# Performance work log

Hardware: AMD Instinct MI355X
Metric: run time of the kernel (lower is better)

## Reference

```python
import jax, jax.numpy as jnp
import numpy as np

H = 16          # n_heads
DH = 128        # head_dim
DR = 64         # rope_dim
DC = DH - DR    # content_dim = 64
THETA = 10000.0
SCALE = 1.0 / np.sqrt(DH)


def _rope_tables(T, dtype):
    inv = 1.0 / (THETA ** (jnp.arange(0, DR, 2, dtype=jnp.float32) / DR))  # [DR/2]
    t = jnp.arange(T, dtype=jnp.float32)
    freqs = jnp.outer(t, inv)  # [T, DR/2]
    return jnp.cos(freqs).astype(dtype), jnp.sin(freqs).astype(dtype)


def _apply_rope(x, cos, sin):
    # x: [B,H,T,DR]; cos/sin: [T,DR/2] broadcast over B,H
    d = x.shape[-1] // 2
    x1, x2 = x[..., :d], x[..., d:]
    return jnp.concatenate([x1 * cos - x2 * sin, x1 * sin + x2 * cos], axis=-1)


def setup_inputs() -> dict:
    key = jax.random.key(0)
    ks = jax.random.split(key, 9)
    B, T, D = 1, 2048, 2048
    s = 0.02
    return {
        "x": jax.random.normal(ks[0], (B, T, D), jnp.float32),
        "Wq_down": jax.random.normal(ks[1], (D, 512), jnp.float32) * s,
        "Wq_up": jax.random.normal(ks[2], (512, H * DC), jnp.float32) * s,
        "Wq_rope": jax.random.normal(ks[3], (D, H * DR), jnp.float32) * s,
        "Wkv_down": jax.random.normal(ks[4], (D, 512), jnp.float32) * s,
        "Wk_up": jax.random.normal(ks[5], (512, H * DC), jnp.float32) * s,
        "Wv_up": jax.random.normal(ks[6], (512, H * DH), jnp.float32) * s,
        "Wk_rope": jax.random.normal(ks[7], (D, H * DR), jnp.float32) * s,
        "Wo": jax.random.normal(ks[8], (H * DH, D), jnp.float32) * s,
    }


def reference(x, Wq_down, Wq_up, Wq_rope, Wkv_down, Wk_up, Wv_up, Wk_rope, Wo):
    B, T, D = x.shape
    # low-rank query path: down then up, content part only
    q_content = ((x @ Wq_down) @ Wq_up).reshape(B, T, H, DC).transpose(0, 2, 1, 3)
    q_pos = (x @ Wq_rope).reshape(B, T, H, DR).transpose(0, 2, 1, 3)
    kv_latent = x @ Wkv_down                    # [B,T,d_latent]
    k_pos = (x @ Wk_rope).reshape(B, T, H, DR).transpose(0, 2, 1, 3)

    cos, sin = _rope_tables(T, x.dtype)
    q_pos = _apply_rope(q_pos, cos, sin)
    k_pos = _apply_rope(k_pos, cos, sin)

    k_content = (kv_latent @ Wk_up).reshape(B, T, H, DC).transpose(0, 2, 1, 3)
    v = (kv_latent @ Wv_up).reshape(B, T, H, DH).transpose(0, 2, 1, 3)

    q = jnp.concatenate([q_content, q_pos], axis=-1)  # [B,H,T,DH]
    k = jnp.concatenate([k_content, k_pos], axis=-1)  # [B,H,T,DH]

    scores = jnp.einsum("bhtd,bhsd->bhts", q, k) * SCALE
    causal = jnp.tril(jnp.ones((T, T), dtype=bool))
    scores = jnp.where(causal, scores, jnp.finfo(scores.dtype).min)
    attn = jax.nn.softmax(scores, axis=-1)
    out = jnp.einsum("bhts,bhsd->bhtd", attn, v)       # [B,H,T,DH]
    out = out.transpose(0, 2, 1, 3).reshape(B, T, H * DH)
    return out @ Wo
```

## Files before the change

### kernel.cpp

```cpp
#include <hip/hip_runtime.h>
#include <math.h>

#define T_SEQ 2048
#define D_MODEL 2048
#define H_HEADS 16
#define DH 128
#define DR 64
#define DC 64
#define D_LAT 512
#define SEGLEN 14
#define NSEG_TOT 46
#define QSCALE (0.08838834764831845f * 1.4426950408889634f)

typedef __attribute__((ext_vector_type(8))) short short8;
typedef __attribute__((ext_vector_type(4))) short short4v;
typedef __attribute__((ext_vector_type(4))) float f32x4;

#if __has_builtin(__builtin_amdgcn_exp2f)
#define EXP2(x) __builtin_amdgcn_exp2f(x)
#else
#define EXP2(x) exp2f(x)
#endif

__device__ __forceinline__ float bf2f(short b) {
    unsigned u = ((unsigned)(unsigned short)b) << 16;
    return __builtin_bit_cast(float, u);
}
__device__ __forceinline__ short f2bf(float f) {
    unsigned u = __builtin_bit_cast(unsigned, f);
    unsigned r = u + 0x7fffu + ((u >> 16) & 1u);
    return (short)(r >> 16);
}
__device__ __forceinline__ short f2bf_trunc(float f) {
    return (short)(__builtin_bit_cast(unsigned, f) >> 16);
}

#define GLD_LDS(gp, lp) \
    __builtin_amdgcn_global_load_lds( \
        (const __attribute__((address_space(1))) void*)(gp), \
        (__attribute__((address_space(3))) void*)(lp), 16, 0, 0)

__device__ __forceinline__ void ct_tile(float (*tile)[33],
                                        const float* __restrict__ W,
                                        short* __restrict__ Wt,
                                        int R, int C, int ldo, int rel) {
    int bx = rel % (C / 32), by = rel / (C / 32);
    int c0 = bx * 32, r0 = by * 32;
    int tx = threadIdx.x & 31, ty = threadIdx.x >> 5;
    #pragma unroll
    for (int i = 0; i < 4; ++i)
        tile[ty + i * 8][tx] = W[(size_t)(r0 + ty + i * 8) * C + c0 + tx];
    __syncthreads();
    #pragma unroll
    for (int i = 0; i < 4; ++i)
        Wt[(size_t)(c0 + ty + i * 8) * ldo + r0 + tx] = f2bf(tile[tx][ty + i * 8]);
    __syncthreads();
}

__global__ __launch_bounds__(256) void prep(const float* __restrict__ x,
                                            short* __restrict__ xb,
                                            const float* __restrict__ Wqd,
                                            const float* __restrict__ Wkvd,
                                            const float* __restrict__ Wqr,
                                            const float* __restrict__ Wkr,
                                            const float* __restrict__ Wqu,
                                            const float* __restrict__ Wku,
                                            const float* __restrict__ Wvu,
                                            const float* __restrict__ Wo,
                                            short* __restrict__ WdT,
                                            short* __restrict__ WupT2,
                                            short* __restrict__ WoT) {
    __shared__ float tile[32][33];
    int bid = blockIdx.x;
    if (bid < 4096) {
        int i = bid * 1024 + threadIdx.x * 4;
        float4 f = *(const float4*)&x[i];
        short4v o;
        o.x = f2bf(f.x); o.y = f2bf(f.y); o.z = f2bf(f.z); o.w = f2bf(f.w);
        *(short4v*)&xb[i] = o;
    } else if (bid < 5120) {
        ct_tile(tile, Wqd,  WdT + (size_t)0 * 2048,    2048, 512,  2048, bid - 4096);
    } else if (bid < 6144) {
        ct_tile(tile, Wkvd, WdT + (size_t)512 * 2048,  2048, 512,  2048, bid - 5120);
    } else if (bid < 8192) {
        ct_tile(tile, Wqr,  WdT + (size_t)1024 * 2048, 2048, 1024, 2048, bid - 6144);
    } else if (bid < 10240) {
        ct_tile(tile, Wkr,  WdT + (size_t)2048 * 2048, 2048, 1024, 2048, bid - 8192);
    } else if (bid < 10752) {
        ct_tile(tile, Wqu,  WupT2 + (size_t)0 * 512,    512, 1024, 512, bid - 10240);
    } else if (bid < 11264) {
        ct_tile(tile, Wku,  WupT2 + (size_t)1024 * 512, 512, 1024, 512, bid - 10752);
    } else if (bid < 12288) {
        ct_tile(tile, Wvu,  WupT2 + (size_t)2048 * 512, 512, 2048, 512, bid - 11264);
    } else {
        ct_tile(tile, Wo,   WoT, 2048, 2048, 2048, bid - 12288);
    }
}

__global__ __launch_bounds__(256) void transpose_bf16(const short* __restrict__ in,
                                                      short* __restrict__ outb,
                                                      int ldi) {
    __shared__ short tile[64][65];
    int c0 = blockIdx.x * 64, t0 = blockIdx.y * 64;
    int tx = threadIdx.x & 31, ty = threadIdx.x >> 5;
    #pragma unroll
    for (int i = 0; i < 8; ++i) {
        int r = ty + i * 8;
        int vv = *(const int*)&in[(size_t)(t0 + r) * ldi + c0 + tx * 2];
        tile[r][tx * 2]     = (short)(vv & 0xffff);
        tile[r][tx * 2 + 1] = (short)(((unsigned)vv) >> 16);
    }
    __syncthreads();
    #pragma unroll
    for (int i = 0; i < 8; ++i) {
        int c = ty + i * 8;
        unsigned lo = (unsigned short)tile[tx * 2][c];
        unsigned hi = (unsigned short)tile[tx * 2 + 1][c];
        *(int*)&outb[(size_t)(c0 + c) * 2048 + t0 + tx * 2] = (int)(lo | (hi << 16));
    }
}

__global__ __launch_bounds__(256) void gemm_bt(const short* __restrict__ A,
                                               const short* __restrict__ A2,
                                               const short* __restrict__ Bt,
                                               short* __restrict__ C0,
                                               short* __restrict__ C1,
                                               short* __restrict__ C2,
                                               short* __restrict__ C3,
                                               int N, int Kblk,
                                               int lda, int ldb, int ldc,
                                               int ncut, int scut, float cscale) {
    __shared__ short As[128 * 32];
    __shared__ short Bs[128 * 32];
    const int tid = threadIdx.x;
    const int wave = tid >> 6, lane = tid & 63;
    const int lin = blockIdx.x;
    const int X = N >> 7, Xq = X >> 2;
    const int xcd = lin & 7;
    int r = lin >> 3;
    const int bx = (xcd & 3) * Xq + (r % Xq); r /= Xq;
    const int by = (xcd >> 2) * 8 + (r & 7);
    const int bz = r >> 3;
    const int row0 = by * 128, col0 = bx * 128;
    const int kbase = bz * Kblk;
    const short* Ause = (col0 < ncut) ? A : A2;
    short* Cuse = (bz == 0) ? C0 : (bz == 1) ? C1 : (bz == 2) ? C2 : C3;
    const int wr = (wave >> 1) * 64, wc = (wave & 1) * 64;
    const int lr = lane & 15, quad = lane >> 4;

    f32x4 acc[4][4];
    #pragma unroll
    for (int i = 0; i < 4; ++i)
        #pragma unroll
        for (int j = 0; j < 4; ++j) acc[i][j] = (f32x4){0.f, 0.f, 0.f, 0.f};

    for (int k0 = kbase; k0 < kbase + Kblk; k0 += 32) {
        __syncthreads();
        #pragma unroll
        for (int it = 0; it < 2; ++it) {
            int idx = wave * 64 + it * 256 + lane;
            const short* ga = Ause + (size_t)(row0 + (idx >> 2)) * lda + k0 + (idx & 3) * 8;
            const short* gb = Bt   + (size_t)(col0 + (idx >> 2)) * ldb + k0 + (idx & 3) * 8;
            int lds0 = (wave * 64 + it * 256) * 8;
            GLD_LDS(ga, &As[lds0]);
            GLD_LDS(gb, &Bs[lds0]);
        }
        __syncthreads();

        short8 af[4], bfr[4];
        #pragma unroll
        for (int i = 0; i < 4; ++i)
            af[i] = *(const short8*)&As[(wr + i * 16 + lr) * 32 + quad * 8];
        #pragma unroll
        for (int j = 0; j < 4; ++j)
            bfr[j] = *(const short8*)&Bs[(wc + j * 16 + lr) * 32 + quad * 8];
        #pragma unroll
        for (int i = 0; i < 4; ++i)
            #pragma unroll
            for (int j = 0; j < 4; ++j)
                acc[i][j] = __builtin_amdgcn_mfma_f32_16x16x32_bf16(af[i], bfr[j],
                                                                   acc[i][j], 0, 0, 0);
    }

    const float sc = (col0 < scut) ? cscale : 1.0f;
    #pragma unroll
    for (int i = 0; i < 4; ++i) {
        int rb = row0 + wr + i * 16 + quad * 4;
        #pragma unroll
        for (int j = 0; j < 4; ++j) {
            int c = col0 + wc + j * 16 + lr;
            #pragma unroll
            for (int rr = 0; rr < 4; ++rr)
                Cuse[(size_t)(rb + rr) * ldc + c] = f2bf(acc[i][j][rr] * sc);
        }
    }
}

__global__ __launch_bounds__(192) void finish_down(short* __restrict__ cat,
                                                   const short* __restrict__ pdown) {
    const int t = blockIdx.x;
    const int k8 = threadIdx.x * 8;
    const int c0 = ((k8 >> 5) << 6) + (k8 & 31);
    const size_t lo = (size_t)t * 3072 + c0;
    const size_t hi = lo + 32;
    short8 al = *(const short8*)&cat[lo];
    short8 ah = *(const short8*)&cat[hi];
    short8 bl = *(const short8*)&pdown[lo];
    short8 bh = *(const short8*)&pdown[hi];
    float xl[8], xh[8];
    #pragma unroll
    for (int j = 0; j < 8; ++j) {
        xl[j] = bf2f(al[j]) + bf2f(bl[j]);
        xh[j] = bf2f(ah[j]) + bf2f(bh[j]);
    }
    if (c0 >= 1024) {
        float sc = (c0 < 2048) ? QSCALE : 1.0f;
        #pragma unroll
        for (int j = 0; j < 8; ++j) {
            int i = (c0 & 31) + j;
            float freq = (float)t * __powf(10000.0f, -(float)i / 32.0f);
            float cs = __cosf(freq), sn = __sinf(freq);
            float r1 = (xl[j] * cs - xh[j] * sn) * sc;
            float r2 = (xl[j] * sn + xh[j] * cs) * sc;
            xl[j] = r1; xh[j] = r2;
        }
    }
    short8 ol, oh;
    #pragma unroll
    for (int j = 0; j < 8; ++j) { ol[j] = f2bf(xl[j]); oh[j] = f2bf(xh[j]); }
    *(short8*)&cat[lo] = ol;
    *(short8*)&cat[hi] = oh;
}

__global__ __launch_bounds__(256) void add_out_f32(const short* __restrict__ p0,
                                                   const short* __restrict__ p1,
                                                   const short* __restrict__ p2,
                                                   const short* __restrict__ p3,
                                                   float* __restrict__ out) {
    int i = (blockIdx.x * 256 + threadIdx.x) * 4;
    short4v a = *(const short4v*)&p0[i];
    short4v b = *(const short4v*)&p1[i];
    short4v c = *(const short4v*)&p2[i];
    short4v d = *(const short4v*)&p3[i];
    float4 o;
    o.x = (bf2f(a.x) + bf2f(b.x)) + (bf2f(c.x) + bf2f(d.x));
    o.y = (bf2f(a.y) + bf2f(b.y)) + (bf2f(c.y) + bf2f(d.y));
    o.z = (bf2f(a.z) + bf2f(b.z)) + (bf2f(c.z) + bf2f(d.z));
    o.w = (bf2f(a.w) + bf2f(b.w)) + (bf2f(c.w) + bf2f(d.w));
    *(float4*)&out[i] = o;
}

__global__ __launch_bounds__(256) void attn_mla_split(const short* __restrict__ qkup,
                                                      const short* __restrict__ cat,
                                                      const short* __restrict__ vT,
                                                      short* __restrict__ slabA,
                                                      short* __restrict__ slabB,
                                                      float* __restrict__ lpart) {
    const int lin = blockIdx.x;
    const int xcd = lin & 7;
    int k_ = lin >> 3;
    const int h = xcd + 8 * (k_ & 1);
    const int pp = k_ >> 1;
    int qt = 0, s = 0, acc = 0;
    #pragma unroll
    for (int q = 0; q < 16; ++q) {
        const int ns = (4 * q + 4 + SEGLEN - 1) / SEGLEN;
        if (pp >= acc) { qt = q; s = pp - acc; }
        acc += ns;
    }
    const int nchunk = 4 * qt + 4;
    const int nsq = (nchunk + SEGLEN - 1) / SEGLEN;
    const int cbase = nchunk / nsq, crem = nchunk % nsq;
    const int c0 = s * cbase + (s < crem ? s : crem);
    const int c1 = c0 + cbase + (s < crem ? 1 : 0);

    const int tid = threadIdx.x;
    const int wave = tid >> 6, lane = tid & 63;
    const int lr = lane & 15, quad = lane >> 4;

    __shared__ short Ks[32 * 128];
    __shared__ short Vst[128 * 32];
    __shared__ short Ps[4][2][16 * 40];

    const short8 ones = {0x3F80, 0x3F80, 0x3F80, 0x3F80,
                         0x3F80, 0x3F80, 0x3F80, 0x3F80};

    const int Q0 = qt * 128;
    const int qrowA = Q0 + wave * 16;
    const int qrowB = qrowA + 64;

    short8 qf[2][4];
    #pragma unroll
    for (int sb = 0; sb < 2; ++sb) {
        int t = (sb ? qrowB : qrowA) + lr;
        #pragma unroll
        for (int kci = 0; kci < 4; ++kci) {
            const short* src = (kci < 2)
                ? qkup + (size_t)t * 4096 + h * 64
                : cat + (size_t)t * 3072 + 1024 + h * 64;
            qf[sb][kci] = *(const short8*)&src[(kci & 1) * 32 + quad * 8];
        }
    }

    const int idx = wave * 64 + lane;
    const int key = idx >> 4;
    const int cg = (idx & 15) ^ (key & 15);
    const short* kp0 = (cg < 8)
        ? qkup + (size_t)key * 4096 + 1024 + h * 64 + cg * 8
        : cat + (size_t)key * 3072 + 2048 + h * 64 + (cg - 8) * 8;
    const int kst = (cg < 8) ? 4096 : 3072;
    const short* kp1 = kp0 + (size_t)16 * kst;
    const int dd = idx >> 2;
    const int scg = (idx & 3) ^ (dd & 3);
    const short* vp0 = vT + (size_t)(h * 128 + dd) * 2048 + scg * 8;
    const short* vp1 = vp0 + (size_t)64 * 2048;
    kp0 += (size_t)c0 * 32 * kst; kp1 += (size_t)c0 * 32 * kst;
    vp0 += c0 * 32;               vp1 += c0 * 32;
    const int kadv = 32 * kst;
    const int vadv = 32;
    const int ldsA = (wave * 64) * 8;
    const int ldsB = (wave * 64 + 256) * 8;

    f32x4 Oacc[2][8];
    #pragma unroll
    for (int sb = 0; sb < 2; ++sb)
        #pragma unroll
        for (int d = 0; d < 8; ++d) Oacc[sb][d] = (f32x4){0.f, 0.f, 0.f, 0.f};
    f32x4 Lacc[2];
    Lacc[0] = (f32x4){0.f, 0.f, 0.f, 0.f};
    Lacc[1] = (f32x4){0.f, 0.f, 0.f, 0.f};

    for (int c = c0; c < c1; ++c) {
        const int s0 = c * 32;
        __syncthreads();
        GLD_LDS(kp0, &Ks[ldsA]);
        GLD_LDS(kp1, &Ks[ldsB]);
        GLD_LDS(vp0, &Vst[ldsA]);
        GLD_LDS(vp1, &Vst[ldsB]);
        kp0 += kadv; kp1 += kadv; vp0 += vadv; vp1 += vadv;
        __syncthreads();
        if (s0 > qrowB + 15) continue;
        const bool actA = (s0 <= qrowA + 15);

        f32x4 sacc[2][2];
        #pragma unroll
        for (int sb = 0; sb < 2; ++sb)
            #pragma unroll
            for (int n = 0; n < 2; ++n) sacc[sb][n] = (f32x4){0.f, 0.f, 0.f, 0.f};
        #pragma unroll
        for (int n = 0; n < 2; ++n) {
            #pragma unroll
            for (int kci = 0; kci < 4; ++kci) {
                short8 kf = *(const short8*)
                    &Ks[(n * 16 + lr) * 128 + ((kci * 4 + quad) ^ lr) * 8];
                if (actA)
                    sacc[0][n] = __builtin_amdgcn_mfma_f32_16x16x32_bf16(
                        qf[0][kci], kf, sacc[0][n], 0, 0, 0);
                sacc[1][n] = __builtin_amdgcn_mfma_f32_16x16x32_bf16(
                    qf[1][kci], kf, sacc[1][n], 0, 0, 0);
            }
        }
        #pragma unroll
        for (int sb = 0; sb < 2; ++sb) {
            if (sb == 0 && !actA) continue;
            const int qrow0 = sb ? qrowB : qrowA;
            if (s0 + 31 > qrow0) {
                #pragma unroll
                for (int r = 0; r < 4; ++r) {
                    int qg = qrow0 + quad * 4 + r;
                    #pragma unroll
                    for (int n = 0; n < 2; ++n) {
                        int sidx = s0 + n * 16 + lr;
                        sacc[sb][n][r] = (sidx <= qg) ? sacc[sb][n][r] : -1e30f;
                    }
                }
            }
            #pragma unroll
            for (int r = 0; r < 4; ++r) {
                Ps[wave][sb][(quad * 4 + r) * 40 + lr] =
                    f2bf_trunc(EXP2(sacc[sb][0][r]));
                Ps[wave][sb][(quad * 4 + r) * 40 + 16 + lr] =
                    f2bf_trunc(EXP2(sacc[sb][1][r]));
            }
        }
        short8 pfA, pfB;
        if (actA) {
            pfA = *(const short8*)&Ps[wave][0][lr * 40 + quad * 8];
            Lacc[0] = __builtin_amdgcn_mfma_f32_16x16x32_bf16(pfA, ones,
                                                              Lacc[0], 0, 0, 0);
        }
        pfB = *(const short8*)&Ps[wave][1][lr * 40 + quad * 8];
        Lacc[1] = __builtin_amdgcn_mfma_f32_16x16x32_bf16(pfB, ones,
                                                          Lacc[1], 0, 0, 0);
        #pragma unroll
        for (int dt = 0; dt < 8; ++dt) {
            short8 vf = *(const short8*)
                &Vst[(dt * 16 + lr) * 32 + (quad ^ (lr & 3)) * 8];
            if (actA)
                Oacc[0][dt] = __builtin_amdgcn_mfma_f32_16x16x32_bf16(
                    pfA, vf, Oacc[0][dt], 0, 0, 0);
            Oacc[1][dt] = __builtin_amdgcn_mfma_f32_16x16x32_bf16(
                pfB, vf, Oacc[1][dt], 0, 0, 0);
        }
    }

    const int slot = h * NSEG_TOT + pp;
    short* slotp = (slot < 512) ? slabA + (size_t)slot * 16384
                                : slabB + (size_t)(slot - 512) * 16384;
    #pragma unroll
    for (int sb = 0; sb < 2; ++sb) {
        const int rbase = wave * 16 + sb * 64 + quad * 4;
        #pragma unroll
        for (int r = 0; r < 4; ++r) {
            #pragma unroll
            for (int dt = 0; dt < 8; ++dt)
                slotp[(rbase + r) * 128 + dt * 16 + lr] = f2bf(Oacc[sb][dt][r]);
        }
        if (lr == 0) {
            #pragma unroll
            for (int r = 0; r < 4; ++r)
                lpart[(size_t)slot * 128 + rbase + r] = Lacc[sb][r];
        }
    }
}

__global__ __launch_bounds__(256) void attn_combine(const short* __restrict__ slabA,
                                                    const short* __restrict__ slabB,
                                                    const float* __restrict__ lpart,
                                                    short* __restrict__ ao) {
    const int t = blockIdx.x;
    const int qt = t >> 7, rl = t & 127;
    const int h = threadIdx.x >> 4;
    const int di = (threadIdx.x & 15) * 8;
    int pf = 0;
    #pragma unroll
    for (int q = 0; q < 16; ++q)
        if (q < qt) pf += (4 * q + 4 + SEGLEN - 1) / SEGLEN;
    const int ns = (4 * qt + 4 + SEGLEN - 1) / SEGLEN;
    float o[8] = {0.f, 0.f, 0.f, 0.f, 0.f, 0.f, 0.f, 0.f};
    float den = 0.f;
    for (int s = 0; s < ns; ++s) {
        const int slot = h * NSEG_TOT + pf + s;
        const short* sp = (slot < 512) ? slabA + (size_t)slot * 16384
                                       : slabB + (size_t)(slot - 512) * 16384;
        short8 v = *(const short8*)&sp[rl * 128 + di];
        #pragma unroll
        for (int j = 0; j < 8; ++j) o[j] += bf2f(v[j]);
        den += lpart[(size_t)slot * 128 + rl];
    }
    float inv = 1.0f / den;
    short8 ov;
    #pragma unroll
    for (int j = 0; j < 8; ++j) ov[j] = f2bf(o[j] * inv);
    *(short8*)&ao[(size_t)t * 2048 + h * 128 + di] = ov;
}

extern "C" void kernel_launch(void* const* d_in, const int* in_sizes, int n_in,
                              void* d_out, int out_size, void* d_ws, size_t ws_size,
                              hipStream_t stream) {
    const float* x        = (const float*)d_in[0];
    const float* Wq_down  = (const float*)d_in[1];
    const float* Wq_up    = (const float*)d_in[2];
    const float* Wq_rope  = (const float*)d_in[3];
    const float* Wkv_down = (const float*)d_in[4];
    const float* Wk_up    = (const float*)d_in[5];
    const float* Wv_up    = (const float*)d_in[6];
    const float* Wk_rope  = (const float*)d_in[7];
    const float* Wo       = (const float*)d_in[8];
    float* out = (float*)d_out;

    short* p = (short*)d_ws;
    short* xb     = p; p += (size_t)2048 * 2048;
    short* WoT    = p; p += (size_t)2048 * 2048;
    short* cat    = p; p += (size_t)2048 * 3072;
    short* upcat2 = p; p += (size_t)2048 * 4096;
    short* WdT    = p; p += (size_t)3072 * 2048;
    short* WupT2  = p; p += (size_t)4096 * 512;
    short* vT     = p; p += (size_t)2048 * 2048;
    float* lpart  = (float*)p;
    short* pdown   = upcat2;
    short* aob     = cat;
    short* slabA   = WdT;
    short* slabB   = xb;
    short* pw0     = upcat2;
    short* pw1     = upcat2 + (size_t)2048 * 2048;
    short* pw2     = WdT;
    short* pw3     = WdT + (size_t)2048 * 2048;

    prep<<<dim3(16384), 256, 0, stream>>>(x, xb, Wq_down, Wkv_down, Wq_rope,
                                          Wk_rope, Wq_up, Wk_up, Wv_up, Wo,
                                          WdT, WupT2, WoT);

    gemm_bt<<<dim3(24 * 16 * 2), 256, 0, stream>>>(xb, xb, WdT, cat, pdown,
                                                   nullptr, nullptr,
                                                   3072, 1024,
                                                   2048, 2048, 3072, 1 << 30, 0, 1.f);

    finish_down<<<dim3(2048), 192, 0, stream>>>(cat, pdown);

    gemm_bt<<<dim3(32 * 16 * 1), 256, 0, stream>>>(cat, cat + 512, WupT2,
                                                   upcat2, nullptr, nullptr, nullptr,
                                                   4096, 512,
                                                   3072, 512, 4096, 1024, 1024, QSCALE);

    transpose_bf16<<<dim3(32, 32), 256, 0, stream>>>(upcat2 + 2048, vT, 4096);

    attn_mla_split<<<dim3(16 * NSEG_TOT), 256, 0, stream>>>(upcat2, cat, vT,
                                                            slabA, slabB, lpart);
    attn_combine<<<dim3(2048), 256, 0, stream>>>(slabA, slabB, lpart, aob);

    gemm_bt<<<dim3(16 * 16 * 4), 256, 0, stream>>>(aob, aob, WoT, pw0, pw1, pw2, pw3,
                                                   2048, 512,
                                                   2048, 2048, 2048, 1 << 30, 0, 1.f);
    add_out_f32<<<dim3(2048 * 2048 / 1024), 256, 0, stream>>>(pw0, pw1, pw2, pw3, out);
}
```

Before: 287.5 us.

## Double-buffer K/V tiles in attention and halve split-K for output GEMM

The attention kernel now double-buffers the K and V LDS tiles. It issues the next chunk's global-to-LDS loads before computing on the current one and waits with explicit vmcnt counters and raw barriers, so load latency overlaps the MFMA work. Separately, the output projection GEMM drops from a 4-way to a 2-way K split, with each partial covering 1024 instead of 512. That halves the partial buffers the reduction kernel reads, at the cost of fewer blocks in that GEMM. The double buffering doubles K/V LDS use, which may lower occupancy.

```diff
diff --git a/kernel.cpp b/kernel.cpp
--- a/kernel.cpp
+++ b/kernel.cpp
@@ -234,19 +234,15 @@
 
 __global__ __launch_bounds__(256) void add_out_f32(const short* __restrict__ p0,
                                                    const short* __restrict__ p1,
-                                                   const short* __restrict__ p2,
-                                                   const short* __restrict__ p3,
                                                    float* __restrict__ out) {
     int i = (blockIdx.x * 256 + threadIdx.x) * 4;
     short4v a = *(const short4v*)&p0[i];
     short4v b = *(const short4v*)&p1[i];
-    short4v c = *(const short4v*)&p2[i];
-    short4v d = *(const short4v*)&p3[i];
     float4 o;
-    o.x = (bf2f(a.x) + bf2f(b.x)) + (bf2f(c.x) + bf2f(d.x));
-    o.y = (bf2f(a.y) + bf2f(b.y)) + (bf2f(c.y) + bf2f(d.y));
-    o.z = (bf2f(a.z) + bf2f(b.z)) + (bf2f(c.z) + bf2f(d.z));
-    o.w = (bf2f(a.w) + bf2f(b.w)) + (bf2f(c.w) + bf2f(d.w));
+    o.x = bf2f(a.x) + bf2f(b.x);
+    o.y = bf2f(a.y) + bf2f(b.y);
+    o.z = bf2f(a.z) + bf2f(b.z);
+    o.w = bf2f(a.w) + bf2f(b.w);
     *(float4*)&out[i] = o;
 }
 
@@ -278,8 +274,8 @@
     const int wave = tid >> 6, lane = tid & 63;
     const int lr = lane & 15, quad = lane >> 4;
 
-    __shared__ short Ks[32 * 128];
-    __shared__ short Vst[128 * 32];
+    __shared__ short Ks[2][32 * 128];
+    __shared__ short Vst[2][128 * 32];
     __shared__ short Ps[4][2][16 * 40];
 
     const short8 ones = {0x3F80, 0x3F80, 0x3F80, 0x3F80,
@@ -330,78 +326,97 @@
     Lacc[0] = (f32x4){0.f, 0.f, 0.f, 0.f};
     Lacc[1] = (f32x4){0.f, 0.f, 0.f, 0.f};
 
+    GLD_LDS(kp0, &Ks[0][ldsA]);
+    GLD_LDS(kp1, &Ks[0][ldsB]);
+    GLD_LDS(vp0, &Vst[0][ldsA]);
+    GLD_LDS(vp1, &Vst[0][ldsB]);
+    kp0 += kadv; kp1 += kadv; vp0 += vadv; vp1 += vadv;
+
+    int cur = 0;
     for (int c = c0; c < c1; ++c) {
         const int s0 = c * 32;
-        __syncthreads();
-        GLD_LDS(kp0, &Ks[ldsA]);
-        GLD_LDS(kp1, &Ks[ldsB]);
-        GLD_LDS(vp0, &Vst[ldsA]);
-        GLD_LDS(vp1, &Vst[ldsB]);
-        kp0 += kadv; kp1 += kadv; vp0 += vadv; vp1 += vadv;
-        __syncthreads();
-        if (s0 > qrowB + 15) continue;
-        const bool actA = (s0 <= qrowA + 15);
-
-        f32x4 sacc[2][2];
-        #pragma unroll
-        for (int sb = 0; sb < 2; ++sb)
-            #pragma unroll
-            for (int n = 0; n < 2; ++n) sacc[sb][n] = (f32x4){0.f, 0.f, 0.f, 0.f};
-        #pragma unroll
-        for (int n = 0; n < 2; ++n) {
-            #pragma unroll
-            for (int kci = 0; kci < 4; ++kci) {
-                short8 kf = *(const short8*)
-                    &Ks[(n * 16 + lr) * 128 + ((kci * 4 + quad) ^ lr) * 8];
-                if (actA)
-                    sacc[0][n] = __builtin_amdgcn_mfma_f32_16x16x32_bf16(
-                        qf[0][kci], kf, sacc[0][n], 0, 0, 0);
-                sacc[1][n] = __builtin_amdgcn_mfma_f32_16x16x32_bf16(
-                    qf[1][kci], kf, sacc[1][n], 0, 0, 0);
+        const bool havenext = (c + 1 < c1);
+        if (havenext) {
+            GLD_LDS(kp0, &Ks[cur ^ 1][ldsA]);
+            GLD_LDS(kp1, &Ks[cur ^ 1][ldsB]);
+            GLD_LDS(vp0, &Vst[cur ^ 1][ldsA]);
+            GLD_LDS(vp1, &Vst[cur ^ 1][ldsB]);
+            kp0 += kadv; kp1 += kadv; vp0 += vadv; vp1 += vadv;
+            asm volatile("s_waitcnt vmcnt(4)" ::: "memory");
+        } else {
+            asm volatile("s_waitcnt vmcnt(0)" ::: "memory");
+        }
+        __builtin_amdgcn_s_barrier();
+
+        if (s0 <= qrowB + 15) {
+            const bool actA = (s0 <= qrowA + 15);
+            const short* Kc = Ks[cur];
+            const short* Vc = Vst[cur];
+
+            f32x4 sacc[2][2];
+            #pragma unroll
+            for (int sb = 0; sb < 2; ++sb)
+                #pragma unroll
+                for (int n = 0; n < 2; ++n) sacc[sb][n] = (f32x4){0.f, 0.f, 0.f, 0.f};
+            #pragma unroll
+            for (int n = 0; n < 2; ++n) {
+                #pragma unroll
+                for (int kci = 0; kci < 4; ++kci) {
+                    short8 kf = *(const short8*)
+                        &Kc[(n * 16 + lr) * 128 + ((kci * 4 + quad) ^ lr) * 8];
+                    if (actA)
+                        sacc[0][n] = __builtin_amdgcn_mfma_f32_16x16x32_bf16(
+                            qf[0][kci], kf, sacc[0][n], 0, 0, 0);
+                    sacc[1][n] = __builtin_amdgcn_mfma_f32_16x16x32_bf16(
+                        qf[1][kci], kf, sacc[1][n], 0, 0, 0);
+                }
             }
-        }
-        #pragma unroll
-        for (int sb = 0; sb < 2; ++sb) {
-            if (sb == 0 && !actA) continue;
-            const int qrow0 = sb ? qrowB : qrowA;
-            if (s0 + 31 > qrow0) {
+            #pragma unroll
+            for (int sb = 0; sb < 2; ++sb) {
+                if (sb == 0 && !actA) continue;
+                const int qrow0 = sb ? qrowB : qrowA;
+                if (s0 + 31 > qrow0) {
+                    #pragma unroll
+                    for (int r = 0; r < 4; ++r) {
+                        int qg = qrow0 + quad * 4 + r;
+                        #pragma unroll
+                        for (int n = 0; n < 2; ++n) {
+                            int sidx = s0 + n * 16 + lr;
+                            sacc[sb][n][r] = (sidx <= qg) ? sacc[sb][n][r] : -1e30f;
+                        }
+                    }
+                }
                 #pragma unroll
                 for (int r = 0; r < 4; ++r) {
-                    int qg = qrow0 + quad * 4 + r;
-                    #pragma unroll
-                    for (int n = 0; n < 2; ++n) {
-                        int sidx = s0 + n * 16 + lr;
-                        sacc[sb][n][r] = (sidx <= qg) ? sacc[sb][n][r] : -1e30f;
-                    }
+                    Ps[wave][sb][(quad * 4 + r) * 40 + lr] =
+                        f2bf_trunc(EXP2(sacc[sb][0][r]));
+                    Ps[wave][sb][(quad * 4 + r) * 40 + 16 + lr] =
+                        f2bf_trunc(EXP2(sacc[sb][1][r]));
                 }
             }
-            #pragma unroll
-            for (int r = 0; r < 4; ++r) {
-                Ps[wave][sb][(quad * 4 + r) * 40 + lr] =
-                    f2bf_trunc(EXP2(sacc[sb][0][r]));
-                Ps[wave][sb][(quad * 4 + r) * 40 + 16 + lr] =
-                    f2bf_trunc(EXP2(sacc[sb][1][r]));
+            short8 pfA, pfB;
+            if (actA) {
+                pfA = *(const short8*)&Ps[wave][0][lr * 40 + quad * 8];
+                Lacc[0] = __builtin_amdgcn_mfma_f32_16x16x32_bf16(pfA, ones,
+                                                                  Lacc[0], 0, 0, 0);
             }
-        }
-        short8 pfA, pfB;
-        if (actA) {
-            pfA = *(const short8*)&Ps[wave][0][lr * 40 + quad * 8];
-            Lacc[0] = __builtin_amdgcn_mfma_f32_16x16x32_bf16(pfA, ones,
-                                                              Lacc[0], 0, 0, 0);
-        }
-        pfB = *(const short8*)&Ps[wave][1][lr * 40 + quad * 8];
-        Lacc[1] = __builtin_amdgcn_mfma_f32_16x16x32_bf16(pfB, ones,
-                                                          Lacc[1], 0, 0, 0);
-        #pragma unroll
-        for (int dt = 0; dt < 8; ++dt) {
-            short8 vf = *(const short8*)
-                &Vst[(dt * 16 + lr) * 32 + (quad ^ (lr & 3)) * 8];
-            if (actA)
-                Oacc[0][dt] = __builtin_amdgcn_mfma_f32_16x16x32_bf16(
-                    pfA, vf, Oacc[0][dt], 0, 0, 0);
-            Oacc[1][dt] = __builtin_amdgcn_mfma_f32_16x16x32_bf16(
-                pfB, vf, Oacc[1][dt], 0, 0, 0);
-        }
+            pfB = *(const short8*)&Ps[wave][1][lr * 40 + quad * 8];
+            Lacc[1] = __builtin_amdgcn_mfma_f32_16x16x32_bf16(pfB, ones,
+                                                              Lacc[1], 0, 0, 0);
+            #pragma unroll
+            for (int dt = 0; dt < 8; ++dt) {
+                short8 vf = *(const short8*)
+                    &Vc[(dt * 16 + lr) * 32 + (quad ^ (lr & 3)) * 8];
+                if (actA)
+                    Oacc[0][dt] = __builtin_amdgcn_mfma_f32_16x16x32_bf16(
+                        pfA, vf, Oacc[0][dt], 0, 0, 0);
+                Oacc[1][dt] = __builtin_amdgcn_mfma_f32_16x16x32_bf16(
+                    pfB, vf, Oacc[1][dt], 0, 0, 0);
+            }
+        }
+
+        __builtin_amdgcn_s_barrier();
+        cur ^= 1;
     }
 
     const int slot = h * NSEG_TOT + pp;
@@ -484,8 +499,6 @@
     short* slabB   = xb;
     short* pw0     = upcat2;
     short* pw1     = upcat2 + (size_t)2048 * 2048;
-    short* pw2     = WdT;
-    short* pw3     = WdT + (size_t)2048 * 2048;
 
     prep<<<dim3(16384), 256, 0, stream>>>(x, xb, Wq_down, Wkv_down, Wq_rope,
                                           Wk_rope, Wq_up, Wk_up, Wv_up, Wo,
@@ -509,8 +522,9 @@
                                                             slabA, slabB, lpart);
     attn_combine<<<dim3(2048), 256, 0, stream>>>(slabA, slabB, lpart, aob);
 
-    gemm_bt<<<dim3(16 * 16 * 4), 256, 0, stream>>>(aob, aob, WoT, pw0, pw1, pw2, pw3,
-                                                   2048, 512,
+    gemm_bt<<<dim3(16 * 16 * 2), 256, 0, stream>>>(aob, aob, WoT, pw0, pw1,
+                                                   nullptr, nullptr,
+                                                   2048, 1024,
                                                    2048, 2048, 2048, 1 << 30, 0, 1.f);
-    add_out_f32<<<dim3(2048 * 2048 / 1024), 256, 0, stream>>>(pw0, pw1, pw2, pw3, out);
-}
+    add_out_f32<<<dim3(2048 * 2048 / 1024), 256, 0, stream>>>(pw0, pw1, out);
+}
```

Result: faster. 278.7 us (-3.1%).
